# Kernel optimization log

Measured on AMD Instinct MI355X. Metric: run time of the kernel, lower is better.

## Reference

```python
import jax, jax.numpy as jnp
import numpy as np

N_NODES = 100000
N_EDGES = 640000
F = 128          # in_features
MID = 192        # (2*F + OUT)//2
OUT = 128


def setup_inputs() -> dict:
    key = jax.random.key(0)
    k_h, k_dr, k_s, k_d, k_w1, k_w2 = jax.random.split(key, 6)
    h = jax.random.normal(k_h, (N_NODES, F), dtype=jnp.float32)
    dR = jax.random.uniform(k_dr, (N_EDGES,), dtype=jnp.float32)
    src_idx = jax.random.randint(k_s, (N_EDGES,), 0, N_NODES)
    dst_idx = jax.random.randint(k_d, (N_EDGES,), 0, N_NODES)
    W1 = jax.random.normal(k_w1, (2 * F + 1, MID), dtype=jnp.float32) * (1.0 / np.sqrt(2 * F + 1))
    b1 = jnp.zeros((MID,), dtype=jnp.float32)
    W2 = jax.random.normal(k_w2, (MID, OUT), dtype=jnp.float32) * (1.0 / np.sqrt(MID))
    b2 = jnp.zeros((OUT,), dtype=jnp.float32)
    return {"h": h, "dR": dR, "src_idx": src_idx, "dst_idx": dst_idx,
            "W1": W1, "b1": b1, "W2": W2, "b2": b2}


def reference(h, dR, src_idx, dst_idx, W1, b1, W2, b2):
    # first=True branch: cat([dst_hidden, src_hidden, dR[:, None]]) -> [E, 2F+1]
    inp = jnp.concatenate([h[dst_idx], h[src_idx], dR[:, None]], axis=1)
    hid = jax.nn.relu(inp @ W1 + b1)          # [E, MID]
    out = jnp.tanh(hid @ W2 + b2)             # [E, OUT]
    return out
```

## Files before the change

### kernel.cpp

```cpp
#include <hip/hip_runtime.h>
#include <hip/hip_bf16.h>


#define F_IN   128
#define MID    192
#define OUT_N  128
#define K1     256
#define M_TILE 64
#define A_STRIDE 264
#define H_STRIDE 200

typedef __attribute__((ext_vector_type(8))) short bf16x8;
typedef __attribute__((ext_vector_type(4))) float f32x4;

__device__ __forceinline__ unsigned short f2bf(float f) {
    unsigned u = __builtin_bit_cast(unsigned, f);
    u = (u + 0x7FFFu + ((u >> 16) & 1u)) >> 16;
    return (unsigned short)u;
}

__global__ void pack_weights(const float* __restrict__ W1,
                             const float* __restrict__ W2,
                             unsigned short* __restrict__ p1,
                             unsigned short* __restrict__ p2,
                             float* __restrict__ wdr) {
    int i = blockIdx.x * 256 + threadIdx.x;
    if (i < K1 * MID) {
        int kin = i & 31;
        int rest = i >> 5;
        int n = rest % MID;
        int kt = rest / MID;
        p1[i] = f2bf(W1[(kt * 32 + kin) * MID + n]);
    }
    int j = i - K1 * MID;
    if (j >= 0 && j < MID * OUT_N) {
        int kin = j & 31;
        int rest = j >> 5;
        int n = rest & 127;
        int kt = rest >> 7;
        p2[j] = f2bf(W2[(kt * 32 + kin) * OUT_N + n]);
    }
    if (i < MID) wdr[i] = W1[256 * MID + i];
}

__global__ __launch_bounds__(256, 4)
void edge_mlp_kernel(const float* __restrict__ h,
                     const float* __restrict__ dR,
                     const int*   __restrict__ src_idx,
                     const int*   __restrict__ dst_idx,
                     const float* __restrict__ b1,
                     const float* __restrict__ b2,
                     const unsigned short* __restrict__ p1,
                     const unsigned short* __restrict__ p2,
                     const float* __restrict__ wdr,
                     float* __restrict__ out) {
    __shared__ __align__(16) unsigned short sA[M_TILE * A_STRIDE];
    __shared__ float sdr[M_TILE];

    const int tid = threadIdx.x;
    const int e0 = blockIdx.x * M_TILE;

    if (tid < M_TILE) sdr[tid] = dR[e0 + tid];

    {
        const int j = tid & 31;
        const int g = tid >> 5;
#pragma unroll
        for (int it = 0; it < 16; ++it) {
            int half = it * 8 + g;
            int e = half >> 1;
            int part = half & 1;
            const int* ip = part ? src_idx : dst_idx;
            int row = ip[e0 + e];
            const float4 v = *(const float4*)(h + (size_t)row * F_IN + j * 4);
            ushort4 b;
            b.x = f2bf(v.x); b.y = f2bf(v.y); b.z = f2bf(v.z); b.w = f2bf(v.w);
            *(ushort4*)(&sA[e * A_STRIDE + part * F_IN + j * 4]) = b;
        }
    }
    __syncthreads();

    const int lane = tid & 63;
    const int w = tid >> 6;
    const int l15 = lane & 15;
    const int q = lane >> 4;

    f32x4 acc1[4][3] = {};
    for (int kt = 0; kt < 8; ++kt) {
        bf16x8 a[4];
#pragma unroll
        for (int m = 0; m < 4; ++m)
            a[m] = *(const bf16x8*)(&sA[(m * 16 + l15) * A_STRIDE + kt * 32 + q * 8]);
#pragma unroll
        for (int ni = 0; ni < 3; ++ni) {
            int nb = (w + ni * 4) * 16 + l15;
            bf16x8 bf = *(const bf16x8*)(&p1[(kt * MID + nb) * 32 + q * 8]);
#pragma unroll
            for (int m = 0; m < 4; ++m)
                acc1[m][ni] = __builtin_amdgcn_mfma_f32_16x16x32_bf16(a[m], bf, acc1[m][ni], 0, 0, 0);
        }
    }
    __syncthreads();

    unsigned short* sH = sA;
#pragma unroll
    for (int ni = 0; ni < 3; ++ni) {
        int n = (w + ni * 4) * 16 + l15;
        float bb = b1[n];
        float wd = wdr[n];
#pragma unroll
        for (int m = 0; m < 4; ++m) {
#pragma unroll
            for (int r = 0; r < 4; ++r) {
                int e = m * 16 + q * 4 + r;
                float v = acc1[m][ni][r] + bb + sdr[e] * wd;
                v = fmaxf(v, 0.0f);
                sH[e * H_STRIDE + n] = f2bf(v);
            }
        }
    }
    __syncthreads();

    f32x4 acc2[4][2] = {};
    for (int kt = 0; kt < 6; ++kt) {
        bf16x8 a[4];
#pragma unroll
        for (int m = 0; m < 4; ++m)
            a[m] = *(const bf16x8*)(&sH[(m * 16 + l15) * H_STRIDE + kt * 32 + q * 8]);
#pragma unroll
        for (int ni = 0; ni < 2; ++ni) {
            int nb = (w + ni * 4) * 16 + l15;
            bf16x8 bf = *(const bf16x8*)(&p2[(kt * OUT_N + nb) * 32 + q * 8]);
#pragma unroll
            for (int m = 0; m < 4; ++m)
                acc2[m][ni] = __builtin_amdgcn_mfma_f32_16x16x32_bf16(a[m], bf, acc2[m][ni], 0, 0, 0);
        }
    }

#pragma unroll
    for (int ni = 0; ni < 2; ++ni) {
        int n = (w + ni * 4) * 16 + l15;
        float bb = b2[n];
#pragma unroll
        for (int m = 0; m < 4; ++m) {
#pragma unroll
            for (int r = 0; r < 4; ++r) {
                int e = e0 + m * 16 + q * 4 + r;
                float x = acc2[m][ni][r] + bb;
                x = fminf(fmaxf(x, -10.0f), 10.0f);
                float t = __expf(2.0f * x);
                out[(size_t)e * OUT_N + n] = (t - 1.0f) * __builtin_amdgcn_rcpf(t + 1.0f);
            }
        }
    }
}

extern "C" void kernel_launch(void* const* d_in, const int* in_sizes, int n_in,
                              void* d_out, int out_size, void* d_ws, size_t ws_size,
                              hipStream_t stream) {
    const float* h   = (const float*)d_in[0];
    const float* dR  = (const float*)d_in[1];
    const int* src   = (const int*)d_in[2];
    const int* dst   = (const int*)d_in[3];
    const float* W1  = (const float*)d_in[4];
    const float* b1  = (const float*)d_in[5];
    const float* W2  = (const float*)d_in[6];
    const float* b2  = (const float*)d_in[7];
    float* out       = (float*)d_out;

    unsigned short* p1 = (unsigned short*)d_ws;
    unsigned short* p2 = p1 + K1 * MID;
    float* wdr         = (float*)(p2 + MID * OUT_N);

    const int E = in_sizes[1];

    pack_weights<<<(K1 * MID + MID * OUT_N + 255) / 256, 256, 0, stream>>>(W1, W2, p1, p2, wdr);
    edge_mlp_kernel<<<E / M_TILE, 256, 0, stream>>>(h, dR, src, dst, b1, b2, p1, p2, wdr, out);
}
```

Measured before the change: 492.6 us.

## Pre-convert node features to bf16 and gather via direct global-to-LDS loads

```diff
diff --git a/kernel.cpp b/kernel.cpp
--- a/kernel.cpp
+++ b/kernel.cpp
@@ -1,5 +1,4 @@
 #include <hip/hip_runtime.h>
-#include <hip/hip_bf16.h>
 
 
 #define F_IN   128
@@ -7,10 +6,10 @@
 #define OUT_N  128
 #define K1     256
 #define M_TILE 64
-#define A_STRIDE 264
 #define H_STRIDE 200
 
 typedef __attribute__((ext_vector_type(8))) short bf16x8;
+typedef __attribute__((ext_vector_type(8))) unsigned short u16x8;
 typedef __attribute__((ext_vector_type(4))) float f32x4;
 
 __device__ __forceinline__ unsigned short f2bf(float f) {
@@ -43,8 +42,21 @@
     if (i < MID) wdr[i] = W1[256 * MID + i];
 }
 
-__global__ __launch_bounds__(256, 4)
-void edge_mlp_kernel(const float* __restrict__ h,
+__global__ void hconv(const float* __restrict__ h,
+                      unsigned short* __restrict__ hb, int n8) {
+    int i = blockIdx.x * 256 + threadIdx.x;
+    if (i >= n8) return;
+    const float4* hp = (const float4*)h;
+    float4 v0 = hp[2 * i];
+    float4 v1 = hp[2 * i + 1];
+    u16x8 o;
+    o[0] = f2bf(v0.x); o[1] = f2bf(v0.y); o[2] = f2bf(v0.z); o[3] = f2bf(v0.w);
+    o[4] = f2bf(v1.x); o[5] = f2bf(v1.y); o[6] = f2bf(v1.z); o[7] = f2bf(v1.w);
+    *((u16x8*)hb + i) = o;
+}
+
+__global__ __launch_bounds__(256, 5)
+void edge_mlp_kernel(const unsigned short* __restrict__ hb,
                      const float* __restrict__ dR,
                      const int*   __restrict__ src_idx,
                      const int*   __restrict__ dst_idx,
@@ -54,47 +66,53 @@
                      const unsigned short* __restrict__ p2,
                      const float* __restrict__ wdr,
                      float* __restrict__ out) {
-    __shared__ __align__(16) unsigned short sA[M_TILE * A_STRIDE];
-    __shared__ float sdr[M_TILE];
-
-    const int tid = threadIdx.x;
-    const int e0 = blockIdx.x * M_TILE;
-
-    if (tid < M_TILE) sdr[tid] = dR[e0 + tid];
+    __shared__ __align__(16) unsigned short sA[M_TILE * 256];
+
+    const int tid  = threadIdx.x;
+    const int lane = tid & 63;
+    const int w    = tid >> 6;
+    const int e0   = blockIdx.x * M_TILE;
+
+    const float dr_own = dR[e0 + lane];
 
     {
-        const int j = tid & 31;
-        const int g = tid >> 5;
-#pragma unroll
-        for (int it = 0; it < 16; ++it) {
-            int half = it * 8 + g;
-            int e = half >> 1;
-            int part = half & 1;
-            const int* ip = part ? src_idx : dst_idx;
-            int row = ip[e0 + e];
-            const float4 v = *(const float4*)(h + (size_t)row * F_IN + j * 4);
-            ushort4 b;
-            b.x = f2bf(v.x); b.y = f2bf(v.y); b.z = f2bf(v.z); b.w = f2bf(v.w);
-            *(ushort4*)(&sA[e * A_STRIDE + part * F_IN + j * 4]) = b;
+        const int g = lane >> 4;
+        const int c = lane & 15;
+        const int part = g & 1;
+        const int* __restrict__ ip = part ? src_idx : dst_idx;
+        const int eb = w * 16 + (g >> 1);
+        int rows[8];
+#pragma unroll
+        for (int i = 0; i < 8; ++i) rows[i] = ip[e0 + eb + 2 * i];
+#pragma unroll
+        for (int i = 0; i < 8; ++i) {
+            const int el = eb + 2 * i;
+            const unsigned short* gp =
+                hb + ((size_t)rows[i] << 7) + ((c ^ (el & 7)) << 3);
+            unsigned short* lp = &sA[(w * 16 + 2 * i) * 256];
+            __builtin_amdgcn_global_load_lds(
+                (const __attribute__((address_space(1))) void*)gp,
+                (__attribute__((address_space(3))) void*)lp,
+                16, 0, 0);
         }
     }
     __syncthreads();
 
-    const int lane = tid & 63;
-    const int w = tid >> 6;
     const int l15 = lane & 15;
-    const int q = lane >> 4;
+    const int q   = lane >> 4;
 
     f32x4 acc1[4][3] = {};
     for (int kt = 0; kt < 8; ++kt) {
         bf16x8 a[4];
 #pragma unroll
-        for (int m = 0; m < 4; ++m)
-            a[m] = *(const bf16x8*)(&sA[(m * 16 + l15) * A_STRIDE + kt * 32 + q * 8]);
+        for (int m = 0; m < 4; ++m) {
+            const int r = m * 16 + l15;
+            a[m] = *(const bf16x8*)(&sA[r * 256 + (((kt * 4 + q) ^ (r & 7)) << 3)]);
+        }
 #pragma unroll
         for (int ni = 0; ni < 3; ++ni) {
-            int nb = (w + ni * 4) * 16 + l15;
-            bf16x8 bf = *(const bf16x8*)(&p1[(kt * MID + nb) * 32 + q * 8]);
+            const int nb = (w + ni * 4) * 16 + l15;
+            bf16x8 bf = *(const bf16x8*)(&p1[((kt * MID + nb) << 5) + (q << 3)]);
 #pragma unroll
             for (int m = 0; m < 4; ++m)
                 acc1[m][ni] = __builtin_amdgcn_mfma_f32_16x16x32_bf16(a[m], bf, acc1[m][ni], 0, 0, 0);
@@ -102,18 +120,25 @@
     }
     __syncthreads();
 
+    float drv[16];
+#pragma unroll
+    for (int m = 0; m < 4; ++m)
+#pragma unroll
+        for (int r = 0; r < 4; ++r)
+            drv[m * 4 + r] = __shfl(dr_own, m * 16 + q * 4 + r);
+
     unsigned short* sH = sA;
 #pragma unroll
     for (int ni = 0; ni < 3; ++ni) {
-        int n = (w + ni * 4) * 16 + l15;
-        float bb = b1[n];
-        float wd = wdr[n];
+        const int n = (w + ni * 4) * 16 + l15;
+        const float bb = b1[n];
+        const float wd = wdr[n];
 #pragma unroll
         for (int m = 0; m < 4; ++m) {
 #pragma unroll
             for (int r = 0; r < 4; ++r) {
-                int e = m * 16 + q * 4 + r;
-                float v = acc1[m][ni][r] + bb + sdr[e] * wd;
+                const int e = m * 16 + q * 4 + r;
+                float v = acc1[m][ni][r] + bb + drv[m * 4 + r] * wd;
                 v = fmaxf(v, 0.0f);
                 sH[e * H_STRIDE + n] = f2bf(v);
             }
@@ -129,8 +154,8 @@
             a[m] = *(const bf16x8*)(&sH[(m * 16 + l15) * H_STRIDE + kt * 32 + q * 8]);
 #pragma unroll
         for (int ni = 0; ni < 2; ++ni) {
-            int nb = (w + ni * 4) * 16 + l15;
-            bf16x8 bf = *(const bf16x8*)(&p2[(kt * OUT_N + nb) * 32 + q * 8]);
+            const int nb = (w + ni * 4) * 16 + l15;
+            bf16x8 bf = *(const bf16x8*)(&p2[((kt * OUT_N + nb) << 5) + (q << 3)]);
 #pragma unroll
             for (int m = 0; m < 4; ++m)
                 acc2[m][ni] = __builtin_amdgcn_mfma_f32_16x16x32_bf16(a[m], bf, acc2[m][ni], 0, 0, 0);
@@ -139,17 +164,18 @@
 
 #pragma unroll
     for (int ni = 0; ni < 2; ++ni) {
-        int n = (w + ni * 4) * 16 + l15;
-        float bb = b2[n];
+        const int n = (w + ni * 4) * 16 + l15;
+        const float bb = b2[n];
 #pragma unroll
         for (int m = 0; m < 4; ++m) {
 #pragma unroll
             for (int r = 0; r < 4; ++r) {
-                int e = e0 + m * 16 + q * 4 + r;
+                const int e = e0 + m * 16 + q * 4 + r;
                 float x = acc2[m][ni][r] + bb;
                 x = fminf(fmaxf(x, -10.0f), 10.0f);
                 float t = __expf(2.0f * x);
-                out[(size_t)e * OUT_N + n] = (t - 1.0f) * __builtin_amdgcn_rcpf(t + 1.0f);
+                float y = (t - 1.0f) * __builtin_amdgcn_rcpf(t + 1.0f);
+                __builtin_nontemporal_store(y, &out[(size_t)e * OUT_N + n]);
             }
         }
     }
@@ -168,12 +194,15 @@
     const float* b2  = (const float*)d_in[7];
     float* out       = (float*)d_out;
 
-    unsigned short* p1 = (unsigned short*)d_ws;
-    unsigned short* p2 = p1 + K1 * MID;
-    float* wdr         = (float*)(p2 + MID * OUT_N);
-
-    const int E = in_sizes[1];
-
+    const int hn = in_sizes[0];
+    const int E  = in_sizes[1];
+
+    unsigned short* hbuf = (unsigned short*)d_ws;
+    unsigned short* p1   = hbuf + hn;
+    unsigned short* p2   = p1 + K1 * MID;
+    float* wdr           = (float*)(p2 + MID * OUT_N);
+
+    hconv<<<(hn / 8 + 255) / 256, 256, 0, stream>>>(h, hbuf, hn / 8);
     pack_weights<<<(K1 * MID + MID * OUT_N + 255) / 256, 256, 0, stream>>>(W1, W2, p1, p2, wdr);
-    edge_mlp_kernel<<<E / M_TILE, 256, 0, stream>>>(h, dR, src, dst, b1, b2, p1, p2, wdr, out);
-}
+    edge_mlp_kernel<<<E / M_TILE, 256, 0, stream>>>(hbuf, dR, src, dst, b1, b2, p1, p2, wdr, out);
+}
```

Measured after the change: 503.9 us. 1.02x slower.
